# Optimization experiments

Hardware: AMD Instinct MI355X
Metric: run time of the kernel (lower is better)

Reference implementation:

```python
import jax, jax.numpy as jnp
import numpy as np

N, E, K_ORDER = 50000, 800000, 3
F_IN, H = 128, 128


def setup_inputs() -> dict:
    key = jax.random.key(0)
    ks = jax.random.split(key, 24)
    s = 0.05
    inp = {
        "x_t": jax.random.normal(ks[0], (N, F_IN), jnp.float32),
        "h_prev": jax.random.normal(ks[1], (N, H), jnp.float32),
        "c_prev": jax.random.normal(ks[2], (N, H), jnp.float32),
        "edge_weight": jax.random.uniform(ks[3], (E,), jnp.float32),
        "edge_index": jax.random.randint(ks[4], (2, E), 0, N, dtype=jnp.int64),
    }
    # Input->gate weight matrices W_* : (F, H)
    for i, nm in enumerate(["W_i", "W_f", "W_c", "W_o"]):
        inp[nm] = jax.random.normal(ks[5 + i], (F_IN, H), jnp.float32) * s
    # ChebConv weights theta_* : (K, H, H) applied to hidden state
    for i, nm in enumerate(["theta_i", "theta_f", "theta_c", "theta_o"]):
        inp[nm] = jax.random.normal(ks[9 + i], (K_ORDER, H, H), jnp.float32) * s
    # Gate biases (b_* of GCLSTM merged with the ChebConv bias; they add)
    for i, nm in enumerate(["b_i", "b_f", "b_c", "b_o"]):
        inp[nm] = jax.random.normal(ks[13 + i], (H,), jnp.float32) * s
    # Peephole weights w_c_* : (H,)
    for i, nm in enumerate(["w_ci", "w_cf", "w_co"]):
        inp[nm] = jax.random.normal(ks[17 + i], (H,), jnp.float32) * s
    return inp


def _cheb_norm(edge_index, edge_weight):
    # get_laplacian('sym') + lambda_max=2 scaling + add_self_loops(-1)
    # => L~ = -D^{-1/2} A D^{-1/2}  (zero diagonal)
    src, dst = edge_index[0], edge_index[1]
    deg = jax.ops.segment_sum(edge_weight, src, num_segments=N)
    dinv = jnp.where(deg > 0, jax.lax.rsqrt(jnp.maximum(deg, 1e-30)), 0.0)
    return src, dst, -edge_weight * dinv[src] * dinv[dst]


def _cheb_conv(x, theta, bias, src, dst, wn):
    # Chebyshev recursion: Tx0=x, Tx1=L~x, Tx_k = 2 L~ Tx_{k-1} - Tx_{k-2}
    def Lmul(v):
        return jax.ops.segment_sum(wn[:, None] * v[src], dst, num_segments=N)
    Tx0 = x
    Tx1 = Lmul(x)
    out = Tx0 @ theta[0] + Tx1 @ theta[1]
    for k in range(2, theta.shape[0]):
        Tx2 = 2.0 * Lmul(Tx1) - Tx0
        out = out + Tx2 @ theta[k]
        Tx0, Tx1 = Tx1, Tx2
    return out + bias


def reference(x_t, h_prev, c_prev, edge_weight, W_i, W_f, W_c, W_o,
              theta_i, theta_f, theta_c, theta_o, b_i, b_f, b_c, b_o,
              w_ci, w_cf, w_co, edge_index):
    src, dst, wn = _cheb_norm(edge_index, edge_weight)
    i = jax.nn.sigmoid(x_t @ W_i + _cheb_conv(h_prev, theta_i, b_i, src, dst, wn)
                       + w_ci * c_prev)
    f = jax.nn.sigmoid(x_t @ W_f + _cheb_conv(h_prev, theta_f, b_f, src, dst, wn)
                       + w_cf * c_prev)
    t = jnp.tanh(x_t @ W_c + _cheb_conv(h_prev, theta_c, b_c, src, dst, wn))
    c_t = f * c_prev + i * t
    o = jax.nn.sigmoid(x_t @ W_o + _cheb_conv(h_prev, theta_o, b_o, src, dst, wn)
                       + w_co * c_t)
    h_t = o * jnp.tanh(c_t)
    return (h_t, c_t)
```

## Files before the change

kernel.cpp:

```cpp
#include <hip/hip_runtime.h>

#define NN 50000
#define EE 800000
#define KC 64
#define EPC (EE / KC)
#define DEG_SCALE 4096.0f
#define NPANEL 782

typedef float f32x4 __attribute__((ext_vector_type(4)));
typedef short bf16x8 __attribute__((ext_vector_type(8)));
typedef unsigned short u16x8 __attribute__((ext_vector_type(8)));

__device__ __forceinline__ unsigned short f2bf(float f) {
  unsigned int u = __float_as_uint(f);
  u += 0x7fffu + ((u >> 16) & 1u);
  return (unsigned short)(u >> 16);
}
__device__ __forceinline__ float bf2f(unsigned short u) {
  return __uint_as_float(((unsigned int)u) << 16);
}

__device__ __forceinline__ void async_copy16(const void* g, void* l) {
  __builtin_amdgcn_global_load_lds(
      (const __attribute__((address_space(1))) unsigned int*)g,
      (__attribute__((address_space(3))) unsigned int*)l, 16, 0, 0);
}

__device__ __forceinline__ float fast_sig(float x) {
  return __builtin_amdgcn_rcpf(1.f + __expf(-x));
}
__device__ __forceinline__ float fast_tanh(float x) {
  return 1.f - 2.f * __builtin_amdgcn_rcpf(__expf(2.f * x) + 1.f);
}

__device__ __forceinline__ unsigned short* hslot2(char* o, long j) {
  return (unsigned short*)(o + (j >> 7) * 512 + (j & 127) * 2);
}
#define CNT_SLOT0 3200000L
#define RANK_SLOT0 3200000L

__global__ __launch_bounds__(1024) void k_pre(
    const float* __restrict__ Wi, const float* __restrict__ Wf,
    const float* __restrict__ Wc, const float* __restrict__ Wo,
    const float* __restrict__ Ti, const float* __restrict__ Tf,
    const float* __restrict__ Tc, const float* __restrict__ To,
    unsigned short* __restrict__ bglob, const float* __restrict__ h,
    const float* __restrict__ x, char* __restrict__ outB,
    const int* __restrict__ src, const int* __restrict__ dst,
    const float* __restrict__ w) {
  const int b = blockIdx.x, tid = threadIdx.x;
  char* cB = outB + (long)NN * 512;
  if (b < KC) {
    __shared__ unsigned histC[12500];
    __shared__ unsigned histD[25000];
    const int base = b * EPC;
    for (int j = tid; j < 12500; j += 1024) histC[j] = 0u;
    for (int j = tid; j < 25000; j += 1024) histD[j] = 0u;
    __syncthreads();
    for (int k = tid; k < EPC; k += 1024) {
      const int e = base + k;
      const int d = dst[e], s = src[e];
      const float wv = w[e];
      const int shc = (d & 3) * 8;
      const unsigned old = atomicAdd(&histC[d >> 2], 1u << shc);
      *hslot2(cB, RANK_SLOT0 + e) = (unsigned short)((old >> shc) & 0xffu);
      const unsigned q = (unsigned)__float2uint_rn(wv * DEG_SCALE);
      atomicAdd(&histD[s >> 1], q << ((s & 1) * 16));
    }
    __syncthreads();
    for (int j = tid; j < 12500; j += 1024) {
      const unsigned v = histC[j];
      const unsigned lo = (v & 0xffu) | (((v >> 8) & 0xffu) << 16);
      const unsigned hi = ((v >> 16) & 0xffu) | (((v >> 24) & 0xffu) << 16);
      uint2 pk; pk.x = lo; pk.y = hi;
      *(uint2*)hslot2(outB, CNT_SLOT0 + (long)b * NN + 4L * j) = pk;
    }
    for (int j = tid; j < 25000; j += 1024)
      *(unsigned*)hslot2(outB, (long)b * NN + 2L * j) = histD[j];
  } else if (b < KC + 32) {
    const int t = (b - KC) * 1024 + tid;
    const int ks = t >> 11;
    const int cf = (t >> 6) & 31;
    const int lane = t & 63;
    const int wv = cf >> 3, hl = (cf >> 2) & 1, g = cf & 3;
    const int kg = lane >> 4, lm = lane & 15;
    const int hc = (wv * 2 + hl) * 16 + lm;
    const float* Wg = (g == 0) ? Wi : (g == 1) ? Wf : (g == 2) ? Wc : Wo;
    const float* Tg = (g == 0) ? Ti : (g == 1) ? Tf : (g == 2) ? Tc : To;
    u16x8 out;
#pragma unroll
    for (int dk = 0; dk < 8; ++dk) {
      const int k = ks * 32 + kg * 8 + dk;
      const int kb = k >> 7, r = k & 127;
      const float v = (kb == 0) ? Wg[r * 128 + hc] : Tg[(kb - 1) * 16384 + r * 128 + hc];
      out[dk] = f2bf(v);
    }
    *(u16x8*)(bglob + t * 8) = out;
  } else if (b < KC + 32 + 782) {
    const int i = (b - (KC + 32)) * 1024 + tid;
    if (i < 100000 * 8) {
      const float* hp = h + i * 8;
      const f32x4 v0 = *(const f32x4*)hp;
      const f32x4 v1 = *(const f32x4*)(hp + 4);
      u16x8 o;
#pragma unroll
      for (int e = 0; e < 4; ++e) o[e] = f2bf(v0[e]);
#pragma unroll
      for (int e = 0; e < 4; ++e) o[e + 4] = f2bf(v1[e]);
      *(u16x8*)(outB + (i >> 4) * 512 + 256 + (i & 15) * 16) = o;
    }
  } else {
    const int i = (b - (KC + 32 + 782)) * 1024 + tid;
    if (i < 100000 * 8) {
      const float* xp = x + i * 8;
      const f32x4 v0 = *(const f32x4*)xp;
      const f32x4 v1 = *(const f32x4*)(xp + 4);
      u16x8 o;
#pragma unroll
      for (int e = 0; e < 4; ++e) o[e] = f2bf(v0[e]);
#pragma unroll
      for (int e = 0; e < 4; ++e) o[e + 4] = f2bf(v1[e]);
      *(u16x8*)(cB + (i >> 4) * 512 + 256 + (i & 15) * 16) = o;
    }
  }
}

__global__ __launch_bounds__(256) void k_phase2(char* __restrict__ outB,
                                                float* __restrict__ dinv,
                                                int* __restrict__ wscnt) {
  char* cB = outB + (long)NN * 512;
  const int lane = threadIdx.x & 63;
  const int i = blockIdx.x * 4 + (threadIdx.x >> 6);
  const int c = lane;
  const int cnt_c = (int)*hslot2(outB, CNT_SLOT0 + (long)c * NN + i);
  const float deg_c = (float)*hslot2(outB, (long)c * NN + i);
  int x = cnt_c;
#pragma unroll
  for (int d = 1; d < 64; d <<= 1) {
    const int y = __shfl_up(x, d, 64);
    if (lane >= d) x += y;
  }
  *hslot2(cB, (long)c * NN + i) = (unsigned short)(x - cnt_c);
  float s = deg_c;
#pragma unroll
  for (int d = 1; d < 64; d <<= 1) s += __shfl_xor(s, d, 64);
  if (lane == 0) {
    s *= (1.0f / DEG_SCALE);
    dinv[i] = (s > 0.f) ? rsqrtf(fmaxf(s, 1e-30f)) : 0.f;
  }
  if (lane == 63) wscnt[i] = x;
}

__device__ __forceinline__ int block_scan_excl_256(int v, int* total) {
  __shared__ int wsum[4];
  const int tid = threadIdx.x;
  const int lane = tid & 63, wv = tid >> 6;
  int x = v;
#pragma unroll
  for (int d = 1; d < 64; d <<= 1) {
    const int y = __shfl_up(x, d, 64);
    if (lane >= d) x += y;
  }
  if (lane == 63) wsum[wv] = x;
  __syncthreads();
  int pre = 0, tot = 0;
#pragma unroll
  for (int u = 0; u < 4; ++u) {
    const int s = wsum[u];
    pre += (u < wv) ? s : 0;
    tot += s;
  }
  *total = tot;
  return pre + x - v;
}

__global__ void k_scan1(const int* __restrict__ wscnt, int* __restrict__ bsum) {
  const int i = blockIdx.x * 256 + threadIdx.x;
  const int v = (i < NN) ? wscnt[i] : 0;
  int tot;
  block_scan_excl_256(v, &tot);
  if (threadIdx.x == 0) bsum[blockIdx.x] = tot;
}

__global__ void k_scan3(const int* __restrict__ wscnt, const int* __restrict__ bsum,
                        int* __restrict__ off) {
  const int tid = threadIdx.x;
  const int vb = (tid < 196 && tid < (int)blockIdx.x) ? bsum[tid] : 0;
  int pre;
  block_scan_excl_256(vb, &pre);
  __syncthreads();
  const int i = blockIdx.x * 256 + tid;
  const int v = (i < NN) ? wscnt[i] : 0;
  int tot;
  const int excl = block_scan_excl_256(v, &tot) + pre;
  if (i < NN) off[i] = excl;
  if (i == NN) off[NN] = excl;
}

__global__ void k_edge2(const int* __restrict__ src, const int* __restrict__ dst,
                        const float* __restrict__ w, const float* __restrict__ dinv,
                        const int* __restrict__ off, char* __restrict__ outB,
                        unsigned* __restrict__ ed) {
  const int e = blockIdx.x * blockDim.x + threadIdx.x;
  if (e >= EE) return;
  char* cB = outB + (long)NN * 512;
  const int s = src[e], d = dst[e];
  const int c = e / EPC;
  const int p = off[d] + (int)*hslot2(cB, (long)c * NN + d) +
                (int)*hslot2(cB, RANK_SLOT0 + e);
  const float wn = -w[e] * dinv[s] * dinv[d];
  ed[p] = (unsigned)s | ((unsigned)f2bf(wn) << 16);
}

__global__ __launch_bounds__(256) void k_gather(
    const char* __restrict__ vinB, const char* __restrict__ vsubB, const float alpha,
    const int* __restrict__ off, const unsigned* __restrict__ ed,
    char* __restrict__ voutB) {
  const int wid = threadIdx.x >> 6, lane = threadIdx.x & 63;
  const int node = blockIdx.x * 4 + wid;
  const int p0 = off[node], p1 = off[node + 1];
  const int lb = lane * 4;
  float ax0 = 0.f, ay0 = 0.f, ax1 = 0.f, ay1 = 0.f;
  float ax2 = 0.f, ay2 = 0.f, ax3 = 0.f, ay3 = 0.f;
  int p = p0;
  for (; p + 7 < p1; p += 8) {
    unsigned E[8];
    unsigned V[8];
#pragma unroll
    for (int u = 0; u < 8; ++u) E[u] = ed[p + u];
#pragma unroll
    for (int u = 0; u < 8; ++u)
      V[u] = *(const unsigned*)(vinB + (long)(E[u] & 0xffffu) * 512 + lb);
#pragma unroll
    for (int u = 0; u < 8; ++u) {
      const float wv = bf2f((unsigned short)(E[u] >> 16));
      float* ax = (u & 3) == 0 ? &ax0 : (u & 3) == 1 ? &ax1 : (u & 3) == 2 ? &ax2 : &ax3;
      float* ay = (u & 3) == 0 ? &ay0 : (u & 3) == 1 ? &ay1 : (u & 3) == 2 ? &ay2 : &ay3;
      *ax = fmaf(wv, bf2f((unsigned short)V[u]), *ax);
      *ay = fmaf(wv, bf2f((unsigned short)(V[u] >> 16)), *ay);
    }
  }
  for (; p + 3 < p1; p += 4) {
    const unsigned e0 = ed[p], e1 = ed[p + 1], e2 = ed[p + 2], e3 = ed[p + 3];
    const unsigned v0 = *(const unsigned*)(vinB + (long)(e0 & 0xffffu) * 512 + lb);
    const unsigned v1 = *(const unsigned*)(vinB + (long)(e1 & 0xffffu) * 512 + lb);
    const unsigned v2 = *(const unsigned*)(vinB + (long)(e2 & 0xffffu) * 512 + lb);
    const unsigned v3 = *(const unsigned*)(vinB + (long)(e3 & 0xffffu) * 512 + lb);
    const float w0 = bf2f((unsigned short)(e0 >> 16)), w1 = bf2f((unsigned short)(e1 >> 16));
    const float w2 = bf2f((unsigned short)(e2 >> 16)), w3 = bf2f((unsigned short)(e3 >> 16));
    ax0 = fmaf(w0, bf2f((unsigned short)v0), ax0);
    ay0 = fmaf(w0, bf2f((unsigned short)(v0 >> 16)), ay0);
    ax1 = fmaf(w1, bf2f((unsigned short)v1), ax1);
    ay1 = fmaf(w1, bf2f((unsigned short)(v1 >> 16)), ay1);
    ax2 = fmaf(w2, bf2f((unsigned short)v2), ax2);
    ay2 = fmaf(w2, bf2f((unsigned short)(v2 >> 16)), ay2);
    ax3 = fmaf(w3, bf2f((unsigned short)v3), ax3);
    ay3 = fmaf(w3, bf2f((unsigned short)(v3 >> 16)), ay3);
  }
  for (; p < p1; ++p) {
    const unsigned e0 = ed[p];
    const unsigned v0 = *(const unsigned*)(vinB + (long)(e0 & 0xffffu) * 512 + lb);
    const float w0 = bf2f((unsigned short)(e0 >> 16));
    ax0 = fmaf(w0, bf2f((unsigned short)v0), ax0);
    ay0 = fmaf(w0, bf2f((unsigned short)(v0 >> 16)), ay0);
  }
  float rx = alpha * ((ax0 + ax1) + (ax2 + ax3));
  float ry = alpha * ((ay0 + ay1) + (ay2 + ay3));
  if (vsubB) {
    const unsigned s = *(const unsigned*)(vsubB + (long)node * 512 + lb);
    rx -= bf2f((unsigned short)s);
    ry -= bf2f((unsigned short)(s >> 16));
  }
  const unsigned ow = (unsigned)f2bf(rx) | ((unsigned)f2bf(ry) << 16);
  *(unsigned*)(voutB + (long)node * 512 + lb) = ow;
}

__global__ __launch_bounds__(512, 4) void k_gemm(
    const char* __restrict__ outB, const unsigned short* __restrict__ bglob,
    const float* __restrict__ c_prev,
    const float* __restrict__ b_i, const float* __restrict__ b_f,
    const float* __restrict__ b_c, const float* __restrict__ b_o,
    const float* __restrict__ w_ci, const float* __restrict__ w_cf,
    const float* __restrict__ w_co, float* __restrict__ h_out,
    float* __restrict__ c_out) {
  __shared__ char lds[65536];
  const int tid = threadIdx.x;
  const int lane = tid & 63;
  const int w = tid >> 6;
  const int kg = lane >> 4;
  const int lm = lane & 15;
  const int m0 = blockIdx.x * 64;

  const char* hB = outB;
  const char* cB = outB + (long)NN * 512;

  {
    const int t8 = tid & 255;
    const int rf = t8 >> 6, ln = t8 & 63;
    const int srow0 = m0 + rf * 16 + (ln & 15);
    const long srow = (srow0 < NN) ? srow0 : (NN - 1);
    const int schunk = (ln >> 4) * 16;
#pragma unroll
    for (int i = 0; i < 8; ++i) {
      const int ks = i * 2 + (tid >> 8);
      const char* base = (ks < 4) ? (cB + 256) : (ks < 8) ? (hB + 256) : (ks < 12) ? hB : cB;
      async_copy16(base + srow * 512 + (ks & 3) * 64 + schunk,
                   &lds[ks * 4096 + t8 * 16]);
    }
  }

  f32x4 acc[16];
#pragma unroll
  for (int i = 0; i < 16; ++i) acc[i] = (f32x4){0.f, 0.f, 0.f, 0.f};

  bf16x8 B[4][4];
  auto loadB = [&](int ks, bf16x8* bb) {
    const unsigned short* fp = bglob + ((ks * 32 + w * 4) * 64 + lane) * 8;
#pragma unroll
    for (int g = 0; g < 4; ++g) bb[g] = *(const bf16x8*)(fp + g * 512);
  };

  loadB(0, B[0]);
  loadB(1, B[1]);
  loadB(2, B[2]);

  __syncthreads();

  const int hc = w * 16 + lm;
  float cp[16];
#pragma unroll
  for (int rf = 0; rf < 4; ++rf)
#pragma unroll
    for (int reg = 0; reg < 4; ++reg) {
      int node = m0 + rf * 16 + kg * 4 + reg;
      if (node >= NN) node = NN - 1;
      cp[rf * 4 + reg] = c_prev[node * 128 + hc];
    }
  loadB(3, B[3]);

#pragma unroll
  for (int ks = 0; ks < 16; ++ks) {
    const int m = ks & 3;
    bf16x8 a[4];
#pragma unroll
    for (int rf = 0; rf < 4; ++rf)
      a[rf] = *(const bf16x8*)(&lds[ks * 4096 + rf * 1024 + lane * 16]);
#pragma unroll
    for (int rf = 0; rf < 4; ++rf)
#pragma unroll
      for (int g = 0; g < 4; ++g)
        acc[rf * 4 + g] =
            __builtin_amdgcn_mfma_f32_16x16x32_bf16(a[rf], B[m][g], acc[rf * 4 + g], 0, 0, 0);
    if (ks + 4 < 16) loadB(ks + 4, B[m]);
  }

  const float bi = b_i[hc], bfv = b_f[hc], bc_ = b_c[hc], bo = b_o[hc];
  const float wci = w_ci[hc], wcf = w_cf[hc], wco = w_co[hc];
#pragma unroll
  for (int rf = 0; rf < 4; ++rf) {
#pragma unroll
    for (int reg = 0; reg < 4; ++reg) {
      const int node = m0 + rf * 16 + kg * 4 + reg;
      if (node < NN) {
        const float cpv = cp[rf * 4 + reg];
        const float pi = acc[rf * 4 + 0][reg] + bi + wci * cpv;
        const float pf = acc[rf * 4 + 1][reg] + bfv + wcf * cpv;
        const float pc = acc[rf * 4 + 2][reg] + bc_;
        const float po = acc[rf * 4 + 3][reg] + bo;
        const float ig = fast_sig(pi);
        const float fg = fast_sig(pf);
        const float ct = fg * cpv + ig * fast_tanh(pc);
        const float og = fast_sig(po + wco * ct);
        h_out[node * 128 + hc] = og * fast_tanh(ct);
        c_out[node * 128 + hc] = ct;
      }
    }
  }
}


extern "C" void kernel_launch(void* const* d_in, const int* in_sizes, int n_in,
                              void* d_out, int out_size, void* d_ws, size_t ws_size,
                              hipStream_t stream) {
  const float* x_t    = (const float*)d_in[0];
  const float* h_prev = (const float*)d_in[1];
  const float* c_prev = (const float*)d_in[2];
  const float* ew     = (const float*)d_in[3];
  const int*   eidx   = (const int*)d_in[4];
  const float* Wi = (const float*)d_in[5];
  const float* Wf = (const float*)d_in[6];
  const float* Wc = (const float*)d_in[7];
  const float* Wo = (const float*)d_in[8];
  const float* Ti = (const float*)d_in[9];
  const float* Tf = (const float*)d_in[10];
  const float* Tc = (const float*)d_in[11];
  const float* To = (const float*)d_in[12];
  const float* bi = (const float*)d_in[13];
  const float* bf = (const float*)d_in[14];
  const float* bc = (const float*)d_in[15];
  const float* bo = (const float*)d_in[16];
  const float* wci = (const float*)d_in[17];
  const float* wcf = (const float*)d_in[18];
  const float* wco = (const float*)d_in[19];

  char* ws = (char*)d_ws;
  float*    dinv  = (float*)(ws + 0);
  int*      wscnt = (int*)(ws + 200192);
  int*      off   = (int*)(ws + 400384);
  int*      bsum  = (int*)(ws + 601088);
  unsigned* ed    = (unsigned*)(ws + 602112);
  unsigned short* bglob = (unsigned short*)(ws + 3802112);

  char* outB = (char*)d_out;
  float* h_out = (float*)d_out;
  float* c_out = h_out + (long)NN * 128;

  const int* esrc = eidx;
  const int* edst = eidx + EE;

  k_pre<<<KC + 32 + 782 + 782, 1024, 0, stream>>>(
      Wi, Wf, Wc, Wo, Ti, Tf, Tc, To, bglob, h_prev, x_t, outB, esrc, edst, ew);
  k_phase2<<<12500, 256, 0, stream>>>(outB, dinv, wscnt);
  k_scan1<<<196, 256, 0, stream>>>(wscnt, bsum);
  k_scan3<<<196, 256, 0, stream>>>(wscnt, bsum, off);
  k_edge2<<<3125, 256, 0, stream>>>(esrc, edst, ew, dinv, off, outB, ed);
  k_gather<<<12500, 256, 0, stream>>>(outB + 256, nullptr, 1.f, off, ed, outB);
  k_gather<<<12500, 256, 0, stream>>>(outB, outB + 256, 2.f, off, ed,
                                      outB + (long)NN * 512);
  k_gemm<<<NPANEL, 512, 0, stream>>>(outB, bglob, c_prev,
                                     bi, bf, bc, bo, wci, wcf, wco, h_out, c_out);
}
```

Before: 189.2 us.

## Fold Chebyshev recurrence into weights and fuse block-sum scan into phase2

Rewrites the Chebyshev output algebraically: Tx2 = 2·L·Tx1 − Tx0 is expanded so the GEMM weights become (theta0 − theta2) for h, theta1 for Tx1 and 2·theta2 for L·Tx1. The second gather then no longer needs the alpha scale or the subtraction read of Tx0. Separately, the per-256-node block sums are accumulated with atomics inside k_phase2, removing the k_scan1 launch at the cost of a memset and contended atomics. The bf16 rounding of intermediates changes slightly because L·Tx1 is stored instead of 2·L·Tx1 − Tx0.

```diff
diff --git a/kernel.cpp b/kernel.cpp
--- a/kernel.cpp
+++ b/kernel.cpp
@@ -92,7 +92,11 @@
     for (int dk = 0; dk < 8; ++dk) {
       const int k = ks * 32 + kg * 8 + dk;
       const int kb = k >> 7, r = k & 127;
-      const float v = (kb == 0) ? Wg[r * 128 + hc] : Tg[(kb - 1) * 16384 + r * 128 + hc];
+      float v;
+      if (kb == 0)      v = Wg[r * 128 + hc];
+      else if (kb == 1) v = Tg[r * 128 + hc] - Tg[2 * 16384 + r * 128 + hc];
+      else if (kb == 2) v = Tg[16384 + r * 128 + hc];
+      else              v = 2.f * Tg[2 * 16384 + r * 128 + hc];
       out[dk] = f2bf(v);
     }
     *(u16x8*)(bglob + t * 8) = out;
@@ -127,7 +131,8 @@
 
 __global__ __launch_bounds__(256) void k_phase2(char* __restrict__ outB,
                                                 float* __restrict__ dinv,
-                                                int* __restrict__ wscnt) {
+                                                int* __restrict__ wscnt,
+                                                int* __restrict__ bsum) {
   char* cB = outB + (long)NN * 512;
   const int lane = threadIdx.x & 63;
   const int i = blockIdx.x * 4 + (threadIdx.x >> 6);
@@ -148,7 +153,10 @@
     s *= (1.0f / DEG_SCALE);
     dinv[i] = (s > 0.f) ? rsqrtf(fmaxf(s, 1e-30f)) : 0.f;
   }
-  if (lane == 63) wscnt[i] = x;
+  if (lane == 63) {
+    wscnt[i] = x;
+    atomicAdd(&bsum[i >> 8], x);
+  }
 }
 
 __device__ __forceinline__ int block_scan_excl_256(int v, int* total) {
@@ -172,14 +180,6 @@
   }
   *total = tot;
   return pre + x - v;
-}
-
-__global__ void k_scan1(const int* __restrict__ wscnt, int* __restrict__ bsum) {
-  const int i = blockIdx.x * 256 + threadIdx.x;
-  const int v = (i < NN) ? wscnt[i] : 0;
-  int tot;
-  block_scan_excl_256(v, &tot);
-  if (threadIdx.x == 0) bsum[blockIdx.x] = tot;
 }
 
 __global__ void k_scan3(const int* __restrict__ wscnt, const int* __restrict__ bsum,
@@ -213,9 +213,8 @@
 }
 
 __global__ __launch_bounds__(256) void k_gather(
-    const char* __restrict__ vinB, const char* __restrict__ vsubB, const float alpha,
-    const int* __restrict__ off, const unsigned* __restrict__ ed,
-    char* __restrict__ voutB) {
+    const char* __restrict__ vinB, const int* __restrict__ off,
+    const unsigned* __restrict__ ed, char* __restrict__ voutB) {
   const int wid = threadIdx.x >> 6, lane = threadIdx.x & 63;
   const int node = blockIdx.x * 4 + wid;
   const int p0 = off[node], p1 = off[node + 1];
@@ -264,13 +263,8 @@
     ax0 = fmaf(w0, bf2f((unsigned short)v0), ax0);
     ay0 = fmaf(w0, bf2f((unsigned short)(v0 >> 16)), ay0);
   }
-  float rx = alpha * ((ax0 + ax1) + (ax2 + ax3));
-  float ry = alpha * ((ay0 + ay1) + (ay2 + ay3));
-  if (vsubB) {
-    const unsigned s = *(const unsigned*)(vsubB + (long)node * 512 + lb);
-    rx -= bf2f((unsigned short)s);
-    ry -= bf2f((unsigned short)(s >> 16));
-  }
+  const float rx = (ax0 + ax1) + (ax2 + ax3);
+  const float ry = (ay0 + ay1) + (ay2 + ay3);
   const unsigned ow = (unsigned)f2bf(rx) | ((unsigned)f2bf(ry) << 16);
   *(unsigned*)(voutB + (long)node * 512 + lb) = ow;
 }
@@ -418,15 +412,14 @@
   const int* esrc = eidx;
   const int* edst = eidx + EE;
 
+  hipMemsetAsync(bsum, 0, 1024, stream);
   k_pre<<<KC + 32 + 782 + 782, 1024, 0, stream>>>(
       Wi, Wf, Wc, Wo, Ti, Tf, Tc, To, bglob, h_prev, x_t, outB, esrc, edst, ew);
-  k_phase2<<<12500, 256, 0, stream>>>(outB, dinv, wscnt);
-  k_scan1<<<196, 256, 0, stream>>>(wscnt, bsum);
+  k_phase2<<<12500, 256, 0, stream>>>(outB, dinv, wscnt, bsum);
   k_scan3<<<196, 256, 0, stream>>>(wscnt, bsum, off);
   k_edge2<<<3125, 256, 0, stream>>>(esrc, edst, ew, dinv, off, outB, ed);
-  k_gather<<<12500, 256, 0, stream>>>(outB + 256, nullptr, 1.f, off, ed, outB);
-  k_gather<<<12500, 256, 0, stream>>>(outB, outB + 256, 2.f, off, ed,
-                                      outB + (long)NN * 512);
+  k_gather<<<12500, 256, 0, stream>>>(outB + 256, off, ed, outB);
+  k_gather<<<12500, 256, 0, stream>>>(outB, off, ed, outB + (long)NN * 512);
   k_gemm<<<NPANEL, 512, 0, stream>>>(outB, bglob, c_prev,
                                      bi, bf, bc, bo, wci, wcf, wco, h_out, c_out);
 }
```

After: 392.5 us. +107.5%, slower.
